# Performance work log

Hardware: AMD Instinct MI355X
Metric: run time of the kernel (lower is better)

Reference implementation:

```python
import jax, jax.numpy as jnp
import numpy as np

N = 500_000      # num nodes
E = 8_000_000    # num edges (before self-loops)
F_IN, H, C = 16, 8, 2


def setup_inputs() -> dict:
    key = jax.random.key(0)
    k = jax.random.split(key, 6)
    x = jax.random.normal(k[0], (N, F_IN), dtype=jnp.float32)
    edge_index = jax.random.randint(k[1], (2, E), 0, N, dtype=jnp.int32)
    # Glorot-style init like PyG GCNConv
    W1 = jax.random.normal(k[2], (F_IN, H), dtype=jnp.float32) * (1.0 / np.sqrt(F_IN))
    b1 = jnp.zeros((H,), dtype=jnp.float32)
    W2 = jax.random.normal(k[3], (H, C), dtype=jnp.float32) * (1.0 / np.sqrt(H))
    b2 = jnp.zeros((C,), dtype=jnp.float32)
    return {"x": x, "W1": W1, "b1": b1, "W2": W2, "b2": b2, "edge_index": edge_index}


def reference(x, W1, b1, W2, b2, edge_index):
    # GCNConv: out = D^{-1/2} (A + I) D^{-1/2} X W + b   (PyG semantics)
    row, col = edge_index[0], edge_index[1]           # messages flow row -> col
    loop = jnp.arange(N, dtype=row.dtype)
    row = jnp.concatenate([row, loop])                # add self-loops
    col = jnp.concatenate([col, loop])
    deg = jax.ops.segment_sum(jnp.ones_like(col, dtype=x.dtype), col, num_segments=N)
    dinv = jnp.where(deg > 0, jax.lax.rsqrt(deg), jnp.zeros_like(deg))
    norm = dinv[row] * dinv[col]                      # [E+N]

    def propagate(h):  # h: [N, d] -> normalized scatter-add aggregation
        msg = h[row] * norm[:, None]                  # gather + scale, [E+N, d]
        return jax.ops.segment_sum(msg, col, num_segments=N)

    h = jax.nn.relu(propagate(x @ W1) + b1)           # [N, 8]
    out = propagate(h @ W2) + b2                      # [N, 2]
    return jax.nn.log_softmax(out, axis=1)
```

## Files before the change

### kernel.cpp

```cpp
#include <hip/hip_runtime.h>

#define TPB 256
#define NBLK_EDGE 512
#define CHUNKE 16384
#define BIN_SHIFT 9
#define BIN_SIZE 512
#define MAXK 1024
#define ROW_BITS 19
#define ROW_MASK ((1u << ROW_BITS) - 1)
#define Q_SHIFT 17
#define NKEY 2048
#define CAP 12288
#define G1_TPB 512
#define SPIN_CAP 20000

typedef _Float16 half8  __attribute__((ext_vector_type(8)));
typedef _Float16 half2v __attribute__((ext_vector_type(2)));

__device__ __forceinline__ int wave_scan_incl(int v, int lane) {
#pragma unroll
    for (int d = 1; d < 64; d <<= 1) {
        int u = __shfl_up(v, d, 64);
        if (lane >= d) v += u;
    }
    return v;
}

__device__ __forceinline__ int block_excl_scan_1024(int v, int tid, int* wsum) {
    int lane = tid & 63, wv = tid >> 6;
    int incl = wave_scan_incl(v, lane);
    if (lane == 63) wsum[wv] = incl;
    __syncthreads();
    if (tid < 16) {
        int w = wsum[tid];
#pragma unroll
        for (int d = 1; d < 16; d <<= 1) {
            int u = __shfl_up(w, d, 16);
            if (tid >= d) w += u;
        }
        wsum[tid] = w;
    }
    __syncthreads();
    return incl - v + (wv ? wsum[wv - 1] : 0);
}

__global__ void __launch_bounds__(1024) k_hist(
        const int* __restrict__ col, int E, int chunk,
        int* __restrict__ cntB, int* __restrict__ cntT) {
    __shared__ int lh[MAXK];
    int blk = blockIdx.x, tid = threadIdx.x;
    lh[tid] = 0;
    __syncthreads();
    int s = blk * chunk, e_ = min(s + chunk, E);
    for (int e = s + tid; e < e_; e += 1024)
        atomicAdd(&lh[col[e] >> BIN_SHIFT], 1);
    __syncthreads();
    int v = lh[tid];
    cntB[(size_t)blk * MAXK + tid] = v;
    cntT[(size_t)tid * NBLK_EDGE + blk] = v;
}

__global__ void k_colscan(int* __restrict__ cntT, int* __restrict__ ghist) {
    __shared__ int part[256];
    int b = blockIdx.x, tid = threadIdx.x;
    size_t base = (size_t)b * NBLK_EDGE;
    int t2 = tid * 2;
    int c0 = cntT[base + t2], c1 = cntT[base + t2 + 1];
    int sum = c0 + c1;
    part[tid] = sum;
    __syncthreads();
    for (int off = 1; off < 256; off <<= 1) {
        int v = (tid >= off) ? part[tid - off] : 0;
        __syncthreads();
        part[tid] += v;
        __syncthreads();
    }
    int excl = part[tid] - sum;
    cntT[base + t2]     = excl;
    cntT[base + t2 + 1] = excl + c0;
    if (tid == 255) ghist[b] = part[255];
}

__global__ void __launch_bounds__(1024) k_scan(
        const int* __restrict__ ghist, int K, int* __restrict__ binBase,
        int* __restrict__ scratchCur, int* __restrict__ barCtr) {
    __shared__ int wsum[16];
    int tid = threadIdx.x;
    if (tid == 0) { *scratchCur = 0; *barCtr = 0; }
    int val = (tid < K) ? ghist[tid] : 0;
    int excl = block_excl_scan_1024(val, tid, wsum);
    binBase[tid] = excl;
    if (tid == K - 1) binBase[K] = excl + val;
}

__global__ void __launch_bounds__(1024) k_reorder(
        const int* __restrict__ row, const int* __restrict__ col,
        int E, int chunk,
        const int* __restrict__ binBase, const int* __restrict__ cntB,
        const int* __restrict__ cntT, unsigned* __restrict__ packed) {
    __shared__ unsigned sorted[CHUNKE];
    __shared__ unsigned short sbin[CHUNKE];
    __shared__ int lcur[MAXK], lbase[MAXK], gbase[MAXK];
    __shared__ int wsum[16];
    int blk = blockIdx.x, tid = threadIdx.x;
    int s = blk * chunk, e_ = min(s + chunk, E), len = e_ - s;
    size_t bb = (size_t)blk * MAXK;
    int c0 = cntB[bb + tid];
    int excl = block_excl_scan_1024(c0, tid, wsum);
    lbase[tid] = excl;
    lcur[tid] = excl;
    gbase[tid] = binBase[tid] + cntT[(size_t)tid * NBLK_EDGE + blk];
    __syncthreads();
    for (int i = tid; i < len; i += blockDim.x) {
        int cc = col[s + i];
        int b = cc >> BIN_SHIFT;
        int slot = atomicAdd(&lcur[b], 1);
        sorted[slot] = ((unsigned)(cc & (BIN_SIZE - 1)) << ROW_BITS) | (unsigned)row[s + i];
        sbin[slot] = (unsigned short)b;
    }
    __syncthreads();
    for (int i = tid; i < len; i += blockDim.x) {
        int b = sbin[i];
        packed[gbase[b] + (i - lbase[b])] = sorted[i];
    }
}

__global__ void __launch_bounds__(1024) k_binsort(
        unsigned* __restrict__ packed, const int* __restrict__ binBase,
        unsigned* __restrict__ scratch, int* __restrict__ scratchCur,
        const float* __restrict__ x, const float* __restrict__ W1,
        half8* __restrict__ g0, int* __restrict__ keyptr, int N, int E, int K) {
    __shared__ unsigned buf2[CAP];
    __shared__ int cnt[NKEY], cur[NKEY];
    __shared__ float w1s[128];
    __shared__ int wsum[16];
    __shared__ int sbShared;
    int tid = threadIdx.x;
    int bin = blockIdx.x;
    int s = binBase[bin], t = binBase[bin + 1];
    int len = t - s;
    bool fast = (len <= CAP);
    cnt[tid] = 0;
    cnt[tid + 1024] = 0;
    if (tid < 128) w1s[tid] = W1[tid];
    if (!fast && tid == 0) sbShared = atomicAdd(scratchCur, len);
    __syncthreads();
    for (int i = tid; i < len; i += 1024) {
        unsigned v = packed[s + i];
        int k = (int)((v >> ROW_BITS) << 2) | (int)((v & ROW_MASK) >> Q_SHIFT);
        atomicAdd(&cnt[k], 1);
    }
    __syncthreads();
    int t2 = tid * 2;
    int c0 = cnt[t2], c1 = cnt[t2 + 1];
    int excl = block_excl_scan_1024(c0 + c1, tid, wsum);
    cur[t2] = excl;
    cur[t2 + 1] = excl + c0;
    int base = bin << BIN_SHIFT;
    if (base + (t2 >> 2) < N) keyptr[((size_t)bin << 11) + t2] = s + excl;
    if (base + ((t2 + 1) >> 2) < N) keyptr[((size_t)bin << 11) + t2 + 1] = s + excl + c0;
    float di = 0.0f;
    int node = base + tid;
    if (tid < BIN_SIZE && node < N) {
        int deg = cnt[4 * tid] + cnt[4 * tid + 1] + cnt[4 * tid + 2] + cnt[4 * tid + 3];
        di = rsqrtf((float)(deg + 1));
    }
    if (bin == K - 1 && tid == 0) keyptr[(size_t)4 * N] = E;
    __syncthreads();
    if (fast) {
        for (int i = tid; i < len; i += 1024) {
            unsigned v = packed[s + i];
            int k = (int)((v >> ROW_BITS) << 2) | (int)((v & ROW_MASK) >> Q_SHIFT);
            int slot = atomicAdd(&cur[k], 1);
            buf2[slot] = v;
        }
        __syncthreads();
        for (int i = tid; i < len; i += 1024) packed[s + i] = buf2[i];
    } else {
        unsigned* stg = scratch + sbShared;
        for (int i = tid; i < len; i += 1024) stg[i] = packed[s + i];
        __threadfence();
        __syncthreads();
        for (int i = tid; i < len; i += 1024) {
            unsigned v = stg[i];
            int k = (int)((v >> ROW_BITS) << 2) | (int)((v & ROW_MASK) >> Q_SHIFT);
            int slot = atomicAdd(&cur[k], 1);
            packed[s + slot] = v;
        }
    }
    if (tid < BIN_SIZE && node < N) {
        const float4* xv = (const float4*)(x + (size_t)node * 16);
        float h[8];
#pragma unroll
        for (int j = 0; j < 8; ++j) h[j] = 0.0f;
#pragma unroll
        for (int kk = 0; kk < 4; ++kk) {
            float4 a = xv[kk];
            int kb = kk * 4;
#pragma unroll
            for (int j = 0; j < 8; ++j)
                h[j] += a.x * w1s[kb * 8 + j] + a.y * w1s[(kb + 1) * 8 + j]
                      + a.z * w1s[(kb + 2) * 8 + j] + a.w * w1s[(kb + 3) * 8 + j];
        }
        half8 g;
#pragma unroll
        for (int j = 0; j < 8; ++j) g[j] = (_Float16)(di * h[j]);
        g0[node] = g;
    }
}

__global__ void __launch_bounds__(G1_TPB, 8) k_gather1(
        const unsigned* __restrict__ packed, const int* __restrict__ keyptr,
        const half8* __restrict__ g0, const float* __restrict__ b1,
        const float* __restrict__ W2, half2v* __restrict__ g1,
        int* __restrict__ barCtr, int nblk, int N) {
    int tid = threadIdx.x;
    int i = blockIdx.x * G1_TPB + tid;
    bool act = (i < N);
    int kp0 = 0, kp1 = 0, kp2 = 0, kp3 = 0, kp4 = 0;
    if (act) {
        int4 k4 = ((const int4*)keyptr)[i];
        kp0 = k4.x; kp1 = k4.y; kp2 = k4.z; kp3 = k4.w;
        kp4 = keyptr[4 * i + 4];
    }
    float acc[8];
#pragma unroll
    for (int j = 0; j < 8; ++j) acc[j] = 0.0f;
#pragma unroll
    for (int q = 0; q < 4; ++q) {
        int e = (q == 0) ? kp0 : (q == 1) ? kp1 : (q == 2) ? kp2 : kp3;
        int t = (q == 0) ? kp1 : (q == 1) ? kp2 : (q == 2) ? kp3 : kp4;
        if (act) {
            for (; e + 4 <= t; e += 4) {
                unsigned p0 = packed[e], p1 = packed[e + 1],
                         p2 = packed[e + 2], p3 = packed[e + 3];
                half8 v0 = g0[p0 & ROW_MASK];
                half8 v1 = g0[p1 & ROW_MASK];
                half8 v2 = g0[p2 & ROW_MASK];
                half8 v3 = g0[p3 & ROW_MASK];
#pragma unroll
                for (int j = 0; j < 8; ++j)
                    acc[j] += (float)v0[j] + (float)v1[j] + (float)v2[j] + (float)v3[j];
            }
            for (; e < t; ++e) {
                half8 v = g0[packed[e] & ROW_MASK];
#pragma unroll
                for (int j = 0; j < 8; ++j) acc[j] += (float)v[j];
            }
        }
        if (q < 3 && nblk > 0) {
            __syncthreads();
            if (tid == 0) {
                __hip_atomic_fetch_add(barCtr, 1, __ATOMIC_RELAXED,
                                       __HIP_MEMORY_SCOPE_AGENT);
                int target = nblk * (q + 1);
                for (int sp = 0; sp < SPIN_CAP; ++sp) {
                    if (__hip_atomic_load(barCtr, __ATOMIC_RELAXED,
                                          __HIP_MEMORY_SCOPE_AGENT) >= target)
                        break;
                    __builtin_amdgcn_s_sleep(2);
                }
            }
            __syncthreads();
        } else {
            __syncthreads();
        }
    }
    if (act) {
        half8 self = g0[i];
        float di = rsqrtf((float)(kp4 - kp0 + 1));
        float o0 = 0.0f, o1 = 0.0f;
#pragma unroll
        for (int j = 0; j < 8; ++j) {
            float hj = fmaxf(di * (acc[j] + (float)self[j]) + b1[j], 0.0f);
            o0 += hj * W2[j * 2 + 0];
            o1 += hj * W2[j * 2 + 1];
        }
        half2v g;
        g.x = (_Float16)(di * o0);
        g.y = (_Float16)(di * o1);
        g1[i] = g;
    }
}

__global__ void __launch_bounds__(TPB) k_gather2(
        const unsigned* __restrict__ packed, const int* __restrict__ keyptr,
        const half2v* __restrict__ g1, const float* __restrict__ b2,
        float* __restrict__ out, int N) {
    int i = blockIdx.x * blockDim.x + threadIdx.x;
    if (i >= N) return;
    int s = keyptr[4 * i], t = keyptr[4 * i + 4];
    half2v sg = g1[i];
    float a0 = (float)sg.x, a1 = (float)sg.y;
    int e = s;
    for (; e + 4 <= t; e += 4) {
        unsigned p0 = packed[e], p1 = packed[e + 1], p2 = packed[e + 2], p3 = packed[e + 3];
        half2v v0 = g1[p0 & ROW_MASK];
        half2v v1 = g1[p1 & ROW_MASK];
        half2v v2 = g1[p2 & ROW_MASK];
        half2v v3 = g1[p3 & ROW_MASK];
        a0 += (float)v0.x + (float)v1.x + (float)v2.x + (float)v3.x;
        a1 += (float)v0.y + (float)v1.y + (float)v2.y + (float)v3.y;
    }
    for (; e < t; ++e) {
        half2v v = g1[packed[e] & ROW_MASK];
        a0 += (float)v.x;
        a1 += (float)v.y;
    }
    float di = rsqrtf((float)(t - s + 1));
    float o0 = di * a0 + b2[0];
    float o1 = di * a1 + b2[1];
    float m = fmaxf(o0, o1);
    float lse = m + logf(expf(o0 - m) + expf(o1 - m));
    ((float2*)out)[i] = make_float2(o0 - lse, o1 - lse);
}

extern "C" void kernel_launch(void* const* d_in, const int* in_sizes, int n_in,
                              void* d_out, int out_size, void* d_ws, size_t ws_size,
                              hipStream_t stream) {
    const float* x  = (const float*)d_in[0];
    const float* W1 = (const float*)d_in[1];
    const float* b1 = (const float*)d_in[2];
    const float* W2 = (const float*)d_in[3];
    const float* b2 = (const float*)d_in[4];
    const int*   ei = (const int*)d_in[5];

    const int N = in_sizes[0] / 16;
    const int E = in_sizes[5] / 2;
    const int* row = ei;
    const int* col = ei + E;
    const int K = (N + BIN_SIZE - 1) >> BIN_SHIFT;

    float* ws   = (float*)d_ws;
    half8* g0   = (half8*)ws;
    half2v* g1  = (half2v*)(ws + (size_t)4 * N);
    unsigned* scratch = (unsigned*)(ws + (size_t)5 * N);
    int* keyptr = (int*)(ws + (size_t)13 * N);
    int*   meta = (int*)(ws + (size_t)17 * N + 8);
    int* ghist      = meta;
    int* binBase    = meta + MAXK;
    int* scratchCur = meta + 2 * MAXK + 16;
    int* barCtr     = meta + 2 * MAXK + 64;
    unsigned* packed = (unsigned*)(meta + 3 * MAXK);
    int* cntB = (int*)(packed + E);
    int* cntT = cntB + (size_t)MAXK * NBLK_EDGE;

    float* out = (float*)d_out;

    const int gN = (N + TPB - 1) / TPB;
    const int g1N = (N + G1_TPB - 1) / G1_TPB;
    const int chunk = (E + NBLK_EDGE - 1) / NBLK_EDGE;

    static int coop_capacity = -1;
    if (coop_capacity < 0) {
        int nb = 0;
        if (hipOccupancyMaxActiveBlocksPerMultiprocessor(&nb, k_gather1,
                                                         G1_TPB, 0) != hipSuccess)
            nb = 0;
        hipDeviceProp_t prop;
        int ncu = 0;
        if (hipGetDeviceProperties(&prop, 0) == hipSuccess) ncu = prop.multiProcessorCount;
        coop_capacity = nb * ncu;
    }
    const int paceN = (coop_capacity >= g1N) ? g1N : 0;

    k_hist   <<<NBLK_EDGE, 1024, 0, stream>>>(col, E, chunk, cntB, cntT);
    k_colscan<<<K, 256, 0, stream>>>(cntT, ghist);
    k_scan   <<<1, MAXK, 0, stream>>>(ghist, K, binBase, scratchCur, barCtr);
    k_reorder<<<NBLK_EDGE, 1024, 0, stream>>>(row, col, E, chunk,
                                              binBase, cntB, cntT, packed);
    k_binsort<<<K, 1024, 0, stream>>>(packed, binBase, scratch, scratchCur,
                                      x, W1, g0, keyptr, N, E, K);
    k_gather1<<<g1N, G1_TPB, 0, stream>>>(packed, keyptr, g0, b1, W2, g1,
                                          barCtr, paceN, N);
    k_gather2<<<gN, TPB, 0, stream>>>(packed, keyptr, g1, b2, out, N);
}
```

Baseline: 342.7 us.

## Split per-node edge gathers across lane groups in both aggregation kernels

The first aggregation kernel now gives each node a group of 4 lanes that stride over its edges, and uses a fixed grid of 1024 blocks where each lane group handles 4 nodes. The paced inter-block barrier is kept, now sized to the fixed grid. The second aggregation kernel now gives each node 16 lanes, which stride over its edges and combine partial sums with shuffle reductions. The aim is to even out the load imbalance from varying node degree and to make neighbouring edge-index reads coalesced. The cost is more threads doing shuffle work, and idle lanes on low-degree nodes.

```diff
diff --git a/kernel.cpp b/kernel.cpp
--- a/kernel.cpp
+++ b/kernel.cpp
@@ -12,6 +12,10 @@
 #define NKEY 2048
 #define CAP 12288
 #define G1_TPB 512
+#define G1_BLOCKS 1024
+#define G1_GRPS (G1_BLOCKS * (G1_TPB / 4))
+#define SLOTS 4
+#define GV_TPB 512
 #define SPIN_CAP 20000
 
 typedef _Float16 half8  __attribute__((ext_vector_type(8)));
@@ -213,47 +217,35 @@
         const unsigned* __restrict__ packed, const int* __restrict__ keyptr,
         const half8* __restrict__ g0, const float* __restrict__ b1,
         const float* __restrict__ W2, half2v* __restrict__ g1,
-        int* __restrict__ barCtr, int nblk, int N) {
+        int* __restrict__ barCtr, int pace, int N) {
     int tid = threadIdx.x;
-    int i = blockIdx.x * G1_TPB + tid;
-    bool act = (i < N);
-    int kp0 = 0, kp1 = 0, kp2 = 0, kp3 = 0, kp4 = 0;
-    if (act) {
-        int4 k4 = ((const int4*)keyptr)[i];
-        kp0 = k4.x; kp1 = k4.y; kp2 = k4.z; kp3 = k4.w;
-        kp4 = keyptr[4 * i + 4];
-    }
-    float acc[8];
-#pragma unroll
-    for (int j = 0; j < 8; ++j) acc[j] = 0.0f;
+    int lane4 = tid & 3;
+    int gid = blockIdx.x * (G1_TPB / 4) + (tid >> 2);
+    float acc[SLOTS][8];
+#pragma unroll
+    for (int s = 0; s < SLOTS; ++s)
+#pragma unroll
+        for (int j = 0; j < 8; ++j) acc[s][j] = 0.0f;
 #pragma unroll
     for (int q = 0; q < 4; ++q) {
-        int e = (q == 0) ? kp0 : (q == 1) ? kp1 : (q == 2) ? kp2 : kp3;
-        int t = (q == 0) ? kp1 : (q == 1) ? kp2 : (q == 2) ? kp3 : kp4;
-        if (act) {
-            for (; e + 4 <= t; e += 4) {
-                unsigned p0 = packed[e], p1 = packed[e + 1],
-                         p2 = packed[e + 2], p3 = packed[e + 3];
-                half8 v0 = g0[p0 & ROW_MASK];
-                half8 v1 = g0[p1 & ROW_MASK];
-                half8 v2 = g0[p2 & ROW_MASK];
-                half8 v3 = g0[p3 & ROW_MASK];
-#pragma unroll
-                for (int j = 0; j < 8; ++j)
-                    acc[j] += (float)v0[j] + (float)v1[j] + (float)v2[j] + (float)v3[j];
+#pragma unroll
+        for (int s = 0; s < SLOTS; ++s) {
+            int node = gid + s * G1_GRPS;
+            if (node < N) {
+                int e0 = keyptr[4 * node + q], e1 = keyptr[4 * node + q + 1];
+                for (int e = e0 + lane4; e < e1; e += 4) {
+                    half8 v = g0[packed[e] & ROW_MASK];
+#pragma unroll
+                    for (int j = 0; j < 8; ++j) acc[s][j] += (float)v[j];
+                }
             }
-            for (; e < t; ++e) {
-                half8 v = g0[packed[e] & ROW_MASK];
-#pragma unroll
-                for (int j = 0; j < 8; ++j) acc[j] += (float)v[j];
-            }
-        }
-        if (q < 3 && nblk > 0) {
+        }
+        if (q < 3 && pace) {
             __syncthreads();
             if (tid == 0) {
                 __hip_atomic_fetch_add(barCtr, 1, __ATOMIC_RELAXED,
                                        __HIP_MEMORY_SCOPE_AGENT);
-                int target = nblk * (q + 1);
+                int target = G1_BLOCKS * (q + 1);
                 for (int sp = 0; sp < SPIN_CAP; ++sp) {
                     if (__hip_atomic_load(barCtr, __ATOMIC_RELAXED,
                                           __HIP_MEMORY_SCOPE_AGENT) >= target)
@@ -262,57 +254,65 @@
                 }
             }
             __syncthreads();
-        } else {
-            __syncthreads();
-        }
-    }
-    if (act) {
-        half8 self = g0[i];
-        float di = rsqrtf((float)(kp4 - kp0 + 1));
-        float o0 = 0.0f, o1 = 0.0f;
+        }
+    }
+#pragma unroll
+    for (int s = 0; s < SLOTS; ++s) {
+        int node = gid + s * G1_GRPS;
+        if (node >= N) continue;
 #pragma unroll
         for (int j = 0; j < 8; ++j) {
-            float hj = fmaxf(di * (acc[j] + (float)self[j]) + b1[j], 0.0f);
-            o0 += hj * W2[j * 2 + 0];
-            o1 += hj * W2[j * 2 + 1];
-        }
-        half2v g;
-        g.x = (_Float16)(di * o0);
-        g.y = (_Float16)(di * o1);
-        g1[i] = g;
-    }
-}
-
-__global__ void __launch_bounds__(TPB) k_gather2(
+            acc[s][j] += __shfl_xor(acc[s][j], 1, 64);
+            acc[s][j] += __shfl_xor(acc[s][j], 2, 64);
+        }
+        if (lane4 == 0) {
+            int kp0 = keyptr[4 * node], kp4 = keyptr[4 * node + 4];
+            half8 self = g0[node];
+            float di = rsqrtf((float)(kp4 - kp0 + 1));
+            float o0 = 0.0f, o1 = 0.0f;
+#pragma unroll
+            for (int j = 0; j < 8; ++j) {
+                float hj = fmaxf(di * (acc[s][j] + (float)self[j]) + b1[j], 0.0f);
+                o0 += hj * W2[j * 2 + 0];
+                o1 += hj * W2[j * 2 + 1];
+            }
+            half2v g;
+            g.x = (_Float16)(di * o0);
+            g.y = (_Float16)(di * o1);
+            g1[node] = g;
+        }
+    }
+}
+
+__global__ void __launch_bounds__(GV_TPB) k_gather2(
         const unsigned* __restrict__ packed, const int* __restrict__ keyptr,
         const half2v* __restrict__ g1, const float* __restrict__ b2,
         float* __restrict__ out, int N) {
-    int i = blockIdx.x * blockDim.x + threadIdx.x;
-    if (i >= N) return;
-    int s = keyptr[4 * i], t = keyptr[4 * i + 4];
-    half2v sg = g1[i];
-    float a0 = (float)sg.x, a1 = (float)sg.y;
-    int e = s;
-    for (; e + 4 <= t; e += 4) {
-        unsigned p0 = packed[e], p1 = packed[e + 1], p2 = packed[e + 2], p3 = packed[e + 3];
-        half2v v0 = g1[p0 & ROW_MASK];
-        half2v v1 = g1[p1 & ROW_MASK];
-        half2v v2 = g1[p2 & ROW_MASK];
-        half2v v3 = g1[p3 & ROW_MASK];
-        a0 += (float)v0.x + (float)v1.x + (float)v2.x + (float)v3.x;
-        a1 += (float)v0.y + (float)v1.y + (float)v2.y + (float)v3.y;
-    }
-    for (; e < t; ++e) {
+    int tid = threadIdx.x;
+    int lane16 = tid & 15;
+    int node = blockIdx.x * (GV_TPB / 16) + (tid >> 4);
+    if (node >= N) return;
+    int s = keyptr[4 * node], t = keyptr[4 * node + 4];
+    float a0 = 0.0f, a1 = 0.0f;
+    for (int e = s + lane16; e < t; e += 16) {
         half2v v = g1[packed[e] & ROW_MASK];
         a0 += (float)v.x;
         a1 += (float)v.y;
     }
-    float di = rsqrtf((float)(t - s + 1));
-    float o0 = di * a0 + b2[0];
-    float o1 = di * a1 + b2[1];
-    float m = fmaxf(o0, o1);
-    float lse = m + logf(expf(o0 - m) + expf(o1 - m));
-    ((float2*)out)[i] = make_float2(o0 - lse, o1 - lse);
+#pragma unroll
+    for (int d = 1; d < 16; d <<= 1) {
+        a0 += __shfl_xor(a0, d, 64);
+        a1 += __shfl_xor(a1, d, 64);
+    }
+    if (lane16 == 0) {
+        half2v self = g1[node];
+        float di = rsqrtf((float)(t - s + 1));
+        float o0 = di * (a0 + (float)self.x) + b2[0];
+        float o1 = di * (a1 + (float)self.y) + b2[1];
+        float m = fmaxf(o0, o1);
+        float lse = m + logf(expf(o0 - m) + expf(o1 - m));
+        ((float2*)out)[node] = make_float2(o0 - lse, o1 - lse);
+    }
 }
 
 extern "C" void kernel_launch(void* const* d_in, const int* in_sizes, int n_in,
@@ -347,8 +347,7 @@
 
     float* out = (float*)d_out;
 
-    const int gN = (N + TPB - 1) / TPB;
-    const int g1N = (N + G1_TPB - 1) / G1_TPB;
+    const int gV = (N + (GV_TPB / 16) - 1) / (GV_TPB / 16);
     const int chunk = (E + NBLK_EDGE - 1) / NBLK_EDGE;
 
     static int coop_capacity = -1;
@@ -362,7 +361,7 @@
         if (hipGetDeviceProperties(&prop, 0) == hipSuccess) ncu = prop.multiProcessorCount;
         coop_capacity = nb * ncu;
     }
-    const int paceN = (coop_capacity >= g1N) ? g1N : 0;
+    const int pace = (coop_capacity >= G1_BLOCKS) ? 1 : 0;
 
     k_hist   <<<NBLK_EDGE, 1024, 0, stream>>>(col, E, chunk, cntB, cntT);
     k_colscan<<<K, 256, 0, stream>>>(cntT, ghist);
@@ -371,7 +370,7 @@
                                               binBase, cntB, cntT, packed);
     k_binsort<<<K, 1024, 0, stream>>>(packed, binBase, scratch, scratchCur,
                                       x, W1, g0, keyptr, N, E, K);
-    k_gather1<<<g1N, G1_TPB, 0, stream>>>(packed, keyptr, g0, b1, W2, g1,
-                                          barCtr, paceN, N);
-    k_gather2<<<gN, TPB, 0, stream>>>(packed, keyptr, g1, b2, out, N);
-}
+    k_gather1<<<G1_BLOCKS, G1_TPB, 0, stream>>>(packed, keyptr, g0, b1, W2, g1,
+                                                barCtr, pace, N);
+    k_gather2<<<gV, GV_TPB, 0, stream>>>(packed, keyptr, g1, b2, out, N);
+}
```

After: 319.3 us. 1.07x faster.
